# Kernel tuning notes

Measured on AMD Instinct MI355X. Metric: run time of the kernel, lower is better.

Reference implementation:

```python
import jax, jax.numpy as jnp
import numpy as np

# ---- constants matching init_kwargs ----
NUM_CLASSES = 20
NUM_GRID = 7
NUM_BBOX = 2
IN_SIZE = 448          # image_shapes = (448, 448)
IOU_THRESHOLD = 0.7    # self.num_threshold passed to batched_nms
SCORE_THRESHOLD = 0.1  # boxes[:, -1] > 0.1 reserve mask
M = NUM_GRID * NUM_GRID  # 49 boxes per image
BATCH = 16384


def setup_inputs() -> dict:
    key = jax.random.key(0)
    out_features = M * (NUM_CLASSES + 5 * NUM_BBOX)  # 1470
    x = jax.random.uniform(key, (BATCH, out_features), dtype=jnp.float32)
    return {"x": x}


def _iou_matrix(boxes):
    # boxes: [M, 4] in (x0, y0, x1, y1). Returns [M, M] pairwise IoU.
    area = jnp.clip(boxes[:, 2] - boxes[:, 0], 0) * jnp.clip(boxes[:, 3] - boxes[:, 1], 0)
    lt = jnp.maximum(boxes[:, None, :2], boxes[None, :, :2])   # [M, M, 2]
    rb = jnp.minimum(boxes[:, None, 2:], boxes[None, :, 2:])   # [M, M, 2]
    wh = jnp.clip(rb - lt, 0)
    inter = wh[..., 0] * wh[..., 1]
    union = area[:, None] + area[None, :] - inter
    return inter / jnp.maximum(union, 1e-9)


def _nms_keep(boxes, scores, labels, valid):
    # Per-image class-aware NMS (torchvision batched_nms semantics via coordinate offsets).
    # boxes [M,4], scores [M], labels [M] int, valid [M] bool -> keep mask [M] bool.
    max_coord = jnp.max(boxes)
    offs = labels.astype(boxes.dtype) * (max_coord + 1.0)
    b = boxes + offs[:, None]
    s = jnp.where(valid, scores, -jnp.inf)
    order = jnp.argsort(-s)                 # descending by score, invalid last
    bs = b[order]
    vs = valid[order]
    iou = _iou_matrix(bs)                   # [M, M]
    idx = jnp.arange(M)

    def step(suppressed, i):
        keep_i = vs[i] & ~suppressed[i]
        suppressed = suppressed | (keep_i & (iou[i] > IOU_THRESHOLD) & (idx > i))
        return suppressed, keep_i

    _, keep_sorted = jax.lax.scan(step, jnp.zeros((M,), bool), idx)
    return jnp.zeros((M,), bool).at[order].set(keep_sorted)


def reference(x):
    N = x.shape[0]
    x = x.reshape(N, M, NUM_CLASSES + 5 * NUM_BBOX)
    class_logits = x[..., :NUM_CLASSES]                       # [N, M, C]
    bb = x[..., NUM_CLASSES:].reshape(N, M, NUM_BBOX, 5)      # [N, M, B, 5]
    # pick the bbox with max confidence per cell
    best = jnp.argmax(bb[..., 4], axis=-1)                    # [N, M]
    yolo_bboxes = jnp.take_along_axis(bb, best[..., None, None], axis=2)[:, :, 0, :]  # [N, M, 5]

    probs = jax.nn.softmax(class_logits, axis=-1)
    labels = jnp.argmax(probs, axis=-1)                       # [N, M]

    # boxes_decode: grid offsets (x tiles, y repeats) then cx/cy/w/h -> corners
    g = jnp.arange(NUM_GRID, dtype=x.dtype)
    x_grid = jnp.tile(g, NUM_GRID)                            # [M]
    y_grid = jnp.repeat(g, NUM_GRID)                          # [M]
    cx = (yolo_bboxes[..., 0] + x_grid) / NUM_GRID
    cy = (yolo_bboxes[..., 1] + y_grid) / NUM_GRID
    hw = yolo_bboxes[..., 2] / 2
    hh = yolo_bboxes[..., 3] / 2
    W = jnp.asarray(IN_SIZE, x.dtype)
    H = jnp.asarray(IN_SIZE, x.dtype)
    x0 = (cx - hw) * W
    y0 = (cy - hh) * H
    x1 = (cx + hw) * W
    y1 = (cy + hh) * H
    scores = yolo_bboxes[..., 4]
    reserve_mask = scores > SCORE_THRESHOLD                   # [N, M]

    # clip_boxes_to_image
    x0 = jnp.clip(x0, 0, IN_SIZE); x1 = jnp.clip(x1, 0, IN_SIZE)
    y0 = jnp.clip(y0, 0, IN_SIZE); y1 = jnp.clip(y1, 0, IN_SIZE)
    boxes = jnp.stack([x0, y0, x1, y1], axis=-1)              # [N, M, 4]

    keep_mask = jax.vmap(_nms_keep)(boxes, scores, labels, reserve_mask)  # [N, M]
    return class_logits, yolo_bboxes, boxes, scores, labels, keep_mask, reserve_mask
```

## Files before the change

kernel.cpp:

```cpp
#include <hip/hip_runtime.h>
#include <math.h>

#define NCLS   20
#define MCELLS 49
#define FEAT   30
#define ITEMF  1470

typedef unsigned long long u64;
typedef unsigned int u32;

__device__ __forceinline__ float bcastf(float v, int l) {
  return __int_as_float(__builtin_amdgcn_readlane(__float_as_int(v), l));
}
__device__ __forceinline__ int bcasti(int v, int l) {
  return __builtin_amdgcn_readlane(v, l);
}

__global__ __launch_bounds__(256) void yolo_post(const float* __restrict__ x,
                                                 float* __restrict__ out,
                                                 int N) {
  const int wave = threadIdx.x >> 6;
  const int lane = threadIdx.x & 63;
  const int n = blockIdx.x * 4 + wave;

  __shared__ float ldsAll[4][ITEMF];

  if (n >= N) return;

  float* L = ldsAll[wave];

  const float2* src = (const float2*)(x) + (size_t)n * (ITEMF / 2);
  float2* Ld = (float2*)L;
#pragma unroll
  for (int i = 0; i < 12; ++i) {
    int idx = lane + i * 64;
    if (idx < ITEMF / 2) Ld[idx] = src[idx];
  }
  __threadfence_block();

  const size_t NM = (size_t)N * MCELLS;
  float* out0 = out;
  float* out1 = out0 + NM * 20;
  float* out2 = out1 + NM * 5;
  float* out3 = out2 + NM * 4;
  float* out4 = out3 + NM;
  float* out5 = out4 + NM;
  float* out6 = out5 + NM;

  {
    float* dst = out0 + (size_t)n * (MCELLS * NCLS);
#pragma unroll
    for (int i = 0; i < 16; ++i) {
      int idx = lane + i * 64;
      if (idx < MCELLS * NCLS) {
        int c = idx / NCLS;
        int k = idx - c * NCLS;
        dst[idx] = L[c * FEAT + k];
      }
    }
  }

  const int m = lane;
  const bool cellv = (m < MCELLS);
  const int base = m * FEAT;

  int   labi = 0;
  float conf = 0.f;
  float x0 = 0.f, y0 = 0.f, x1 = 0.f, y1 = 0.f;
  bool reserve = false;

  if (cellv) {
    float bestv = L[base];
#pragma unroll
    for (int c = 1; c < NCLS; ++c) {
      float v = L[base + c];
      if (v > bestv) { bestv = v; labi = c; }
    }

    float c0 = L[base + 24], c1 = L[base + 29];
    int bsel = (c1 > c0) ? 1 : 0;
    int bb = base + NCLS + bsel * 5;
    float bx = L[bb], by = L[bb + 1], bw = L[bb + 2], bh = L[bb + 3];
    conf = L[bb + 4];

    float xg = (float)(m % 7), yg = (float)(m / 7);
    float cx = (bx + xg) / 7.0f, cy = (by + yg) / 7.0f;
    float hw = bw * 0.5f, hh = bh * 0.5f;
    x0 = fminf(fmaxf((cx - hw) * 448.0f, 0.f), 448.f);
    y0 = fminf(fmaxf((cy - hh) * 448.0f, 0.f), 448.f);
    x1 = fminf(fmaxf((cx + hw) * 448.0f, 0.f), 448.f);
    y1 = fminf(fmaxf((cy + hh) * 448.0f, 0.f), 448.f);
    reserve = (conf > 0.1f);

    size_t ci = (size_t)n * MCELLS + m;
    float* yb = out1 + ci * 5;
    yb[0] = bx; yb[1] = by; yb[2] = bw; yb[3] = bh; yb[4] = conf;
    *(float4*)(out2 + ci * 4) = make_float4(x0, y0, x1, y1);
    out3[ci] = conf;
    out4[ci] = (float)labi;
    out6[ci] = reserve ? 1.0f : 0.0f;
  }

  bool vld0 = cellv && reserve;
  u64 key;
  if (vld0) {
    u32 sb = __float_as_uint(conf);
    u32 inv = 0x7FFFFFFFu - sb;
    key = ((u64)labi << 37) | ((u64)inv << 6) | (u64)lane;
  } else {
    key = ~0ull;
  }

#pragma unroll
  for (int k = 2; k <= 64; k <<= 1) {
#pragma unroll
    for (int j = k >> 1; j >= 1; j >>= 1) {
      u64 ok = __shfl(key, lane ^ j);
      bool lower = (lane & j) == 0;
      bool asc = (lane & k) == 0;
      if ((key > ok) == (lower == asc)) key = ok;
    }
  }

  const int sid = (int)(key & 63);
  const bool valid = (key != ~0ull);
  const int slab = (int)((key >> 37) & 31);

  float gx0 = __shfl(x0, sid), gy0 = __shfl(y0, sid);
  float gx1 = __shfl(x1, sid), gy1 = __shfl(y1, sid);
  float garea = fmaxf(gx1 - gx0, 0.f) * fmaxf(gy1 - gy0, 0.f);

  u64 rowm = 0;
  for (int d = 1; d < MCELLS; ++d) {
    int src = (lane + d) & 63;
    int plab = __shfl(slab, src);
    bool match = (plab == slab);
    u64 anyreal = __ballot(match && (slab != 31) && (lane + d < 64));
    if (anyreal == 0) break;
    float px0 = __shfl(gx0, src), py0 = __shfl(gy0, src);
    float px1 = __shfl(gx1, src), py1 = __shfl(gy1, src);
    float pa  = bcastf(garea, 0) * 0.f + __shfl(garea, src);
    float iw = fmaxf(fminf(px1, gx1) - fmaxf(px0, gx0), 0.f);
    float ih = fmaxf(fminf(py1, gy1) - fmaxf(py0, gy0), 0.f);
    float inter = iw * ih;
    float uni = pa + garea - inter;
    bool ok = match && (inter > 0.7f * fmaxf(uni, 1e-9f));
    rowm |= ok ? (1ull << src) : 0ull;
  }

  u64 vmask = __ballot(valid);
  int V = __popcll(vmask);
  u64 supp = 0, keep = 0;
  int rlo = (int)(rowm & 0xFFFFFFFFull);
  int rhi = (int)(rowm >> 32);
  for (int i = 0; i < V; ++i) {
    if (!((supp >> i) & 1ull)) {
      keep |= 1ull << i;
      u64 rm = ((u64)(u32)bcasti(rhi, i) << 32) | (u32)bcasti(rlo, i);
      supp |= rm;
    }
  }

  int keepbit = (int)((keep >> lane) & 1ull);
  int kf = __builtin_amdgcn_ds_permute(sid << 2, __float_as_int((float)keepbit));
  if (cellv) out5[(size_t)n * MCELLS + m] = __int_as_float(kf);
}

extern "C" void kernel_launch(void* const* d_in, const int* in_sizes, int n_in,
                              void* d_out, int out_size, void* d_ws, size_t ws_size,
                              hipStream_t stream) {
  const float* x = (const float*)d_in[0];
  float* out = (float*)d_out;
  int N = in_sizes[0] / ITEMF;
  int grid = (N + 3) / 4;
  yolo_post<<<grid, 256, 0, stream>>>(x, out, N);
}
```

Before: 42.17 us.

## Load cells directly to registers, bound IoU loop by segment length, use nontemporal stores

Drops the LDS staging buffer: each lane loads its own 30-float cell into registers as float2 vectors, and the class-logit copy reads straight from global memory. The pairwise IoU loop now runs for a trip count taken from the longest same-label run in the sorted order, replacing the per-iteration ballot early-exit. The greedy NMS walks only the unsuppressed rows via ctz instead of visiting every valid index. All outputs use nontemporal stores to avoid polluting cache. The cost is uncoalesced per-lane strided global loads (120-byte stride) and a second read of the logits from global memory.

```diff
diff --git a/kernel.cpp b/kernel.cpp
--- a/kernel.cpp
+++ b/kernel.cpp
@@ -8,13 +8,12 @@
 
 typedef unsigned long long u64;
 typedef unsigned int u32;
+typedef float f32x4 __attribute__((ext_vector_type(4)));
 
-__device__ __forceinline__ float bcastf(float v, int l) {
-  return __int_as_float(__builtin_amdgcn_readlane(__float_as_int(v), l));
-}
 __device__ __forceinline__ int bcasti(int v, int l) {
   return __builtin_amdgcn_readlane(v, l);
 }
+__device__ __forceinline__ void nts(float* p, float v) { __builtin_nontemporal_store(v, p); }
 
 __global__ __launch_bounds__(256) void yolo_post(const float* __restrict__ x,
                                                  float* __restrict__ out,
@@ -22,21 +21,9 @@
   const int wave = threadIdx.x >> 6;
   const int lane = threadIdx.x & 63;
   const int n = blockIdx.x * 4 + wave;
-
-  __shared__ float ldsAll[4][ITEMF];
-
   if (n >= N) return;
 
-  float* L = ldsAll[wave];
-
-  const float2* src = (const float2*)(x) + (size_t)n * (ITEMF / 2);
-  float2* Ld = (float2*)L;
-#pragma unroll
-  for (int i = 0; i < 12; ++i) {
-    int idx = lane + i * 64;
-    if (idx < ITEMF / 2) Ld[idx] = src[idx];
-  }
-  __threadfence_block();
+  const float* item = x + (size_t)n * ITEMF;
 
   const size_t NM = (size_t)N * MCELLS;
   float* out0 = out;
@@ -47,6 +34,19 @@
   float* out5 = out4 + NM;
   float* out6 = out5 + NM;
 
+  const int m = lane;
+  const bool cellv = (m < MCELLS);
+
+  float2 v[15];
+  if (cellv) {
+    const float2* Lp = (const float2*)(item + m * FEAT);
+#pragma unroll
+    for (int j = 0; j < 15; ++j) v[j] = Lp[j];
+  } else {
+#pragma unroll
+    for (int j = 0; j < 15; ++j) v[j] = make_float2(0.f, 0.f);
+  }
+
   {
     float* dst = out0 + (size_t)n * (MCELLS * NCLS);
 #pragma unroll
@@ -55,33 +55,32 @@
       if (idx < MCELLS * NCLS) {
         int c = idx / NCLS;
         int k = idx - c * NCLS;
-        dst[idx] = L[c * FEAT + k];
+        nts(dst + idx, item[c * FEAT + k]);
       }
     }
   }
 
-  const int m = lane;
-  const bool cellv = (m < MCELLS);
-  const int base = m * FEAT;
-
   int   labi = 0;
   float conf = 0.f;
   float x0 = 0.f, y0 = 0.f, x1 = 0.f, y1 = 0.f;
-  bool reserve = false;
+  bool  reserve = false;
 
   if (cellv) {
-    float bestv = L[base];
+    float bestv = v[0].x;
+    if (v[0].y > bestv) { bestv = v[0].y; labi = 1; }
 #pragma unroll
-    for (int c = 1; c < NCLS; ++c) {
-      float v = L[base + c];
-      if (v > bestv) { bestv = v; labi = c; }
+    for (int j = 1; j < 10; ++j) {
+      if (v[j].x > bestv) { bestv = v[j].x; labi = 2 * j; }
+      if (v[j].y > bestv) { bestv = v[j].y; labi = 2 * j + 1; }
     }
 
-    float c0 = L[base + 24], c1 = L[base + 29];
-    int bsel = (c1 > c0) ? 1 : 0;
-    int bb = base + NCLS + bsel * 5;
-    float bx = L[bb], by = L[bb + 1], bw = L[bb + 2], bh = L[bb + 3];
-    conf = L[bb + 4];
+    float c0 = v[12].x, c1 = v[14].y;
+    bool sel1 = (c1 > c0);
+    float bx = sel1 ? v[12].y : v[10].x;
+    float by = sel1 ? v[13].x : v[10].y;
+    float bw = sel1 ? v[13].y : v[11].x;
+    float bh = sel1 ? v[14].x : v[11].y;
+    conf = sel1 ? c1 : c0;
 
     float xg = (float)(m % 7), yg = (float)(m / 7);
     float cx = (bx + xg) / 7.0f, cy = (by + yg) / 7.0f;
@@ -94,16 +93,16 @@
 
     size_t ci = (size_t)n * MCELLS + m;
     float* yb = out1 + ci * 5;
-    yb[0] = bx; yb[1] = by; yb[2] = bw; yb[3] = bh; yb[4] = conf;
-    *(float4*)(out2 + ci * 4) = make_float4(x0, y0, x1, y1);
-    out3[ci] = conf;
-    out4[ci] = (float)labi;
-    out6[ci] = reserve ? 1.0f : 0.0f;
+    nts(yb + 0, bx); nts(yb + 1, by); nts(yb + 2, bw); nts(yb + 3, bh); nts(yb + 4, conf);
+    f32x4 bx4 = { x0, y0, x1, y1 };
+    __builtin_nontemporal_store(bx4, (f32x4*)(out2 + ci * 4));
+    nts(out3 + ci, conf);
+    nts(out4 + ci, (float)labi);
+    nts(out6 + ci, reserve ? 1.0f : 0.0f);
   }
 
-  bool vld0 = cellv && reserve;
   u64 key;
-  if (vld0) {
+  if (cellv && reserve) {
     u32 sb = __float_as_uint(conf);
     u32 inv = 0x7FFFFFFFu - sb;
     key = ((u64)labi << 37) | ((u64)inv << 6) | (u64)lane;
@@ -122,48 +121,60 @@
     }
   }
 
-  const int sid = (int)(key & 63);
-  const bool valid = (key != ~0ull);
+  const int sid  = (int)(key & 63);
   const int slab = (int)((key >> 37) & 31);
 
   float gx0 = __shfl(x0, sid), gy0 = __shfl(y0, sid);
   float gx1 = __shfl(x1, sid), gy1 = __shfl(y1, sid);
   float garea = fmaxf(gx1 - gx0, 0.f) * fmaxf(gy1 - gy0, 0.f);
 
+  {
+  }
+  int prevlab = __shfl(slab, (lane + 63) & 63);
+  bool rstart = (lane == 0) || (prevlab != slab);
+  u64 S = __ballot(rstart);
+  u64 le_mask = (lane == 63) ? ~0ull : ((2ull << lane) - 1ull);
+  int st = 63 - __builtin_clzll(S & le_mask);
+  u64 gt = (lane == 63) ? 0ull : (S >> (lane + 1));
+  int nxt = gt ? (lane + 1 + (int)__builtin_ctzll(gt)) : 64;
+  int rl = (slab != 31) ? (nxt - st) : 1;
+#pragma unroll
+  for (int d2 = 1; d2 < 64; d2 <<= 1) {
+    int o = __shfl_xor(rl, d2);
+    rl = rl > o ? rl : o;
+  }
+  const int Dmax = __builtin_amdgcn_readfirstlane(rl);
+
   u64 rowm = 0;
-  for (int d = 1; d < MCELLS; ++d) {
-    int src = (lane + d) & 63;
-    int plab = __shfl(slab, src);
-    bool match = (plab == slab);
-    u64 anyreal = __ballot(match && (slab != 31) && (lane + d < 64));
-    if (anyreal == 0) break;
-    float px0 = __shfl(gx0, src), py0 = __shfl(gy0, src);
-    float px1 = __shfl(gx1, src), py1 = __shfl(gy1, src);
-    float pa  = bcastf(garea, 0) * 0.f + __shfl(garea, src);
+  for (int d = 1; d < Dmax; ++d) {
+    int srcl = (lane + d) & 63;
+    int plab = __shfl(slab, srcl);
+    float px0 = __shfl(gx0, srcl), py0 = __shfl(gy0, srcl);
+    float px1 = __shfl(gx1, srcl), py1 = __shfl(gy1, srcl);
+    float pa  = __shfl(garea, srcl);
+    bool match = (plab == slab) && (slab != 31) && (lane + d < 64);
     float iw = fmaxf(fminf(px1, gx1) - fmaxf(px0, gx0), 0.f);
     float ih = fmaxf(fminf(py1, gy1) - fmaxf(py0, gy0), 0.f);
     float inter = iw * ih;
     float uni = pa + garea - inter;
     bool ok = match && (inter > 0.7f * fmaxf(uni, 1e-9f));
-    rowm |= ok ? (1ull << src) : 0ull;
+    rowm |= ok ? (1ull << srcl) : 0ull;
   }
 
-  u64 vmask = __ballot(valid);
-  int V = __popcll(vmask);
-  u64 supp = 0, keep = 0;
-  int rlo = (int)(rowm & 0xFFFFFFFFull);
-  int rhi = (int)(rowm >> 32);
-  for (int i = 0; i < V; ++i) {
-    if (!((supp >> i) & 1ull)) {
-      keep |= 1ull << i;
-      u64 rm = ((u64)(u32)bcasti(rhi, i) << 32) | (u32)bcasti(rlo, i);
-      supp |= rm;
-    }
+  int V = __popcll(__ballot(key != ~0ull));
+  int rlo = (int)(rowm & 0xFFFFFFFFull), rhi = (int)(rowm >> 32);
+  u64 remaining = (V >= 64) ? ~0ull : ((1ull << V) - 1ull);
+  u64 keep = 0;
+  while (remaining) {
+    int i = (int)__builtin_ctzll(remaining);
+    keep |= 1ull << i;
+    u64 rm = ((u64)(u32)bcasti(rhi, i) << 32) | (u32)bcasti(rlo, i);
+    remaining &= ~(rm | (1ull << i));
   }
 
-  int keepbit = (int)((keep >> lane) & 1ull);
-  int kf = __builtin_amdgcn_ds_permute(sid << 2, __float_as_int((float)keepbit));
-  if (cellv) out5[(size_t)n * MCELLS + m] = __int_as_float(kf);
+  int kb = (int)((keep >> lane) & 1ull);
+  int kf = __builtin_amdgcn_ds_permute(sid << 2, __float_as_int((float)kb));
+  if (cellv) nts(out5 + (size_t)n * MCELLS + m, __int_as_float(kf));
 }
 
 extern "C" void kernel_launch(void* const* d_in, const int* in_sizes, int n_in,
```

Result: slower. 43.09 us (+2.2%).
